# Optimization experiments

Hardware: AMD Instinct MI355X
Metric: run time of the kernel (lower is better)

## Reference

```python
import jax, jax.numpy as jnp
import numpy as np

B, N, E, K, DI, DO = 16, 1024, 16, 3, 32, 32


def setup_inputs() -> dict:
    key = jax.random.key(0)
    k1, k2, k3, k4, k5 = jax.random.split(key, 5)
    return {
        "x": jax.random.normal(k1, (B, N, DI), dtype=jnp.float32),
        "all_emb": jax.random.normal(k2, (B, N, E), dtype=jnp.float32),
        "stock_emb": jax.random.normal(k3, (B, N, E), dtype=jnp.float32),
        "weights_pool": jax.random.normal(k4, (E, K, DI, DO), dtype=jnp.float32) * 0.1,
        "bias_pool": jax.random.normal(k5, (E, DO), dtype=jnp.float32) * 0.1,
    }


def reference(x, all_emb, stock_emb, weights_pool, bias_pool):
    # dynamic adjacency: relu(E E^T) then row softmax -> [B, N, N]
    A = jax.nn.relu(jnp.einsum('bne,bme->bnm', all_emb, all_emb))
    S = jax.nn.softmax(A, axis=-1)
    b, n, _ = S.shape
    k_orders = weights_pool.shape[1]
    eye = jnp.broadcast_to(jnp.eye(n, dtype=S.dtype), S.shape)
    # Chebyshev recursion T_0 = I, T_1 = S, T_k = 2 S T_{k-1} - T_{k-2}
    supports = [eye, S]
    for _ in range(2, k_orders):
        supports.append(2.0 * jnp.matmul(S, supports[-1]) - supports[-2])
    cheby = jnp.stack(supports, axis=1)  # [B, K, N, N]
    # graph propagation per Chebyshev order: [B, K, N, dim_in]
    x_g = jnp.einsum('bkij,bjd->bkid', cheby, x)
    # node-specific weights from stock_emb, fused with conv (avoids [B,N,K,I,O]):
    # original: weights = einsum('bni,ikop->bnkop'); out = einsum('bkni,bnkio->bnko').sum(k)
    out = jnp.einsum('bkni,bne,ekio->bno', x_g, stock_emb, weights_pool)
    bias = jnp.einsum('bne,eo->bno', stock_emb, bias_pool)
    return out + bias
```

## Files before the change

### kernel.cpp

```cpp
#include <hip/hip_runtime.h>
#include <stdint.h>

typedef __bf16 bf16x8 __attribute__((ext_vector_type(8)));
typedef __bf16 bf16x4 __attribute__((ext_vector_type(4)));
typedef float  f32x16 __attribute__((ext_vector_type(16)));

constexpr int kB = 16;
constexpr int kN = 1024;
constexpr int kE = 16;

struct bfhl { __bf16 h, l; };
__device__ __forceinline__ bfhl hilo(float v) {
    bfhl r;
    r.h = (__bf16)v;
    r.l = (__bf16)(v - (float)r.h);
    return r;
}

__global__ __launch_bounds__(256) void prep(
    const float* __restrict__ emb, const float* __restrict__ x,
    const float* __restrict__ Wp,
    __bf16* __restrict__ es, __bf16* __restrict__ vt1,
    __bf16* __restrict__ xgb, __bf16* __restrict__ wq)
{
    __shared__ float ls[64 * 33];
    const int tid = threadIdx.x;
    const int bid = blockIdx.x;

    if (bid < 256) {
        int c = bid * 256 + tid;
        int row = c >> 2, seg = c & 3;
        float4 v = *(const float4*)(emb + (size_t)c * 4);
        float f[4] = {v.x, v.y, v.z, v.w};
        bf16x4 hi, lo;
        #pragma unroll
        for (int i = 0; i < 4; ++i) { bfhl t = hilo(f[i]); hi[i] = t.h; lo[i] = t.l; }
        __bf16* r = es + (size_t)row * 32;
        *(bf16x4*)(r + seg * 4)      = hi;
        *(bf16x4*)(r + 16 + seg * 4) = lo;
    } else if (bid < 512) {
        const int bb = bid - 256;
        const int b = bb >> 4, n0 = (bb & 15) << 6;
        const float* sB = x + ((size_t)b * kN + n0) * 32;
        #pragma unroll
        for (int it = 0; it < 2; ++it) {
            int f = it * 256 + tid;
            int row = f >> 3, q8 = f & 7;
            float4 v = *(const float4*)(sB + (size_t)row * 32 + q8 * 4);
            ls[row * 33 + q8 * 4 + 0] = v.x;
            ls[row * 33 + q8 * 4 + 1] = v.y;
            ls[row * 33 + q8 * 4 + 2] = v.z;
            ls[row * 33 + q8 * 4 + 3] = v.w;
        }
        __syncthreads();
        if (tid < 128) {
            const int d = (tid >> 2) & 31, ng = tid & 3;
            bf16x8 o0, o1;
            #pragma unroll
            for (int i = 0; i < 16; ++i) {
                __bf16 hcast = (__bf16)ls[(ng * 16 + i) * 33 + d];
                if (i < 8) o0[i] = hcast; else o1[i - 8] = hcast;
            }
            __bf16* dp = vt1 + (size_t)b * 65536 + (size_t)d * 1024 + n0 + ng * 16;
            *(bf16x8*)dp       = o0;
            *(bf16x8*)(dp + 8) = o1;
        }
        {
            const int r2 = tid >> 2, jg = tid & 3;
            bf16x8 hi, lo;
            #pragma unroll
            for (int i = 0; i < 8; ++i) {
                bfhl t = hilo(ls[r2 * 33 + jg * 8 + i]);
                hi[i] = t.h; lo[i] = t.l;
            }
            __bf16* dp = xgb + (size_t)(b * kN + n0 + r2) * 192 + jg * 8;
            *(bf16x8*)dp        = hi;
            *(bf16x8*)(dp + 96) = lo;
        }
    } else {
        int idx = (bid - 512) * 256 + tid;
        if (idx < 6144) {
            int e = idx / 384, rem = idx - e * 384;
            int ks = rem / 64, r2 = rem - ks * 64;
            int o = r2 >> 1, h = r2 & 1;
            int ki0 = ks * 16 + h * 8;
            bf16x8 hi;
            #pragma unroll
            for (int j = 0; j < 8; ++j)
                hi[j] = (__bf16)Wp[(size_t)e * 3072 + (size_t)(ki0 + j) * 32 + o];
            *(bf16x8*)(wq + (size_t)(e * 6 + ks) * 512 + o * 16 + h * 8) = hi;
        }
    }
}

template<int STAGE>
__global__ __launch_bounds__(256, 2) void apply_mfma(
    const __bf16* __restrict__ es,
    const __bf16* __restrict__ vtin,
    const float*  __restrict__ x,
    __bf16* __restrict__ vt2,
    __bf16* __restrict__ xgb)
{
    __shared__ __bf16 es_s[256 * 40];
    __shared__ __bf16 vt_s[32 * 264];
    __shared__ float  ps[4 * 32 * 33];
    __shared__ float  Ls[4 * 32];
    __shared__ float  yb[32 * 33];

    const int tid = threadIdx.x;
    const int w = tid >> 6, l = tid & 63;
    const int q = l & 31, h = l >> 5;
    const int b = blockIdx.x >> 5, q0 = (blockIdx.x & 31) << 5;

    const __bf16* esB = es + (size_t)b * 32768;
    const __bf16* vtB = vtin + (size_t)b * 65536;

    const __bf16* qr = esB + (size_t)(q0 + q) * 32;
    bf16x8 bhi = *(const bf16x8*)(qr + 8 * h);
    bf16x8 blo = *(const bf16x8*)(qr + 16 + 8 * h);

    f32x16 acc = {};
    float Lp = 0.f;

    for (int ch = 0; ch < 4; ++ch) {
        __syncthreads();
        #pragma unroll
        for (int i = 0; i < 4; ++i) {
            int f = i * 256 + tid;
            int rl = f >> 2, c = f & 3;
            bf16x8 v = *(const bf16x8*)(esB + (size_t)(ch * 256 + rl) * 32 + c * 8);
            *(bf16x8*)(es_s + rl * 40 + c * 8) = v;
        }
        #pragma unroll
        for (int it = 0; it < 2; ++it) {
            int G = it * 256 + tid;
            int d = G >> 4, g = G & 15;
            const __bf16* src = vtB + (size_t)d * 1024 + ch * 256 + g * 16;
            bf16x8 in0 = *(const bf16x8*)src;
            bf16x8 in1 = *(const bf16x8*)(src + 8);
            bf16x8 out0 = __builtin_shufflevector(in0, in1, 0, 1, 2, 3, 8, 9, 10, 11);
            bf16x8 out1 = __builtin_shufflevector(in0, in1, 4, 5, 6, 7, 12, 13, 14, 15);
            *(bf16x8*)(vt_s + d * 264 + g * 16)     = out0;
            *(bf16x8*)(vt_s + d * 264 + g * 16 + 8) = out1;
        }
        __syncthreads();

        #pragma unroll
        for (int sub = 0; sub < 2; ++sub) {
            const int kbl = (w << 6) + (sub << 5);
            const __bf16* ar = es_s + (size_t)(kbl + q) * 40;
            bf16x8 ahi = *(const bf16x8*)(ar + 8 * h);
            bf16x8 alo = *(const bf16x8*)(ar + 16 + 8 * h);

            f32x16 S = {};
            S = __builtin_amdgcn_mfma_f32_32x32x16_bf16(ahi, bhi, S, 0, 0, 0);
            S = __builtin_amdgcn_mfma_f32_32x32x16_bf16(ahi, blo, S, 0, 0, 0);
            S = __builtin_amdgcn_mfma_f32_32x32x16_bf16(alo, bhi, S, 0, 0, 0);

            float p[16];
            #pragma unroll
            for (int r = 0; r < 16; ++r) {
                p[r] = __expf(fmaxf(S[r], 0.f));
                Lp += p[r];
            }
            bf16x8 P0, P1;
            #pragma unroll
            for (int j = 0; j < 8; ++j) { P0[j] = (__bf16)p[j]; P1[j] = (__bf16)p[8 + j]; }

            const __bf16* vh = vt_s + (size_t)q * 264 + kbl;
            bf16x8 A0 = *(const bf16x8*)(vh + 8 * h);
            bf16x8 A1 = *(const bf16x8*)(vh + 16 + 8 * h);
            acc = __builtin_amdgcn_mfma_f32_32x32x16_bf16(A0, P0, acc, 0, 0, 0);
            acc = __builtin_amdgcn_mfma_f32_32x32x16_bf16(A1, P1, acc, 0, 0, 0);
        }
    }

    Lp += __shfl_xor(Lp, 32);
    #pragma unroll
    for (int r = 0; r < 16; ++r) {
        int d = (r & 3) + 8 * (r >> 2) + 4 * h;
        ps[w * 1056 + d * 33 + q] = acc[r];
    }
    if (l < 32) Ls[w * 32 + l] = Lp;
    __syncthreads();

    const int qq = tid >> 3, dg = tid & 7;
    const float iL = 1.f / (Ls[qq] + Ls[32 + qq] + Ls[64 + qq] + Ls[96 + qq]);
    float yv[4];
    #pragma unroll
    for (int i = 0; i < 4; ++i) {
        int d = dg * 4 + i;
        yv[i] = (ps[d * 33 + qq] + ps[1056 + d * 33 + qq] +
                 ps[2112 + d * 33 + qq] + ps[3168 + d * 33 + qq]) * iL;
    }

    {
        float src[4];
        if (STAGE == 2) {
            float4 xv = *(const float4*)(x + (size_t)(b * kN + q0 + qq) * 32 + dg * 4);
            src[0] = 2.f * yv[0] - xv.x; src[1] = 2.f * yv[1] - xv.y;
            src[2] = 2.f * yv[2] - xv.z; src[3] = 2.f * yv[3] - xv.w;
        } else {
            #pragma unroll
            for (int i = 0; i < 4; ++i) src[i] = yv[i];
        }
        const int koff = (STAGE == 1) ? 32 : 64;
        bf16x4 hi, lo;
        #pragma unroll
        for (int i = 0; i < 4; ++i) { bfhl t = hilo(src[i]); hi[i] = t.h; lo[i] = t.l; }
        __bf16* dp = xgb + (size_t)(b * kN + q0 + qq) * 192 + koff + dg * 4;
        *(bf16x4*)dp        = hi;
        *(bf16x4*)(dp + 96) = lo;
    }

    if (STAGE == 1) {
        #pragma unroll
        for (int i = 0; i < 4; ++i) yb[qq * 33 + dg * 4 + i] = yv[i];
        __syncthreads();
        const int d = tid >> 3, qg = tid & 7;
        bf16x4 hi;
        #pragma unroll
        for (int i = 0; i < 4; ++i) hi[i] = (__bf16)yb[(qg * 4 + i) * 33 + d];
        *(bf16x4*)(vt2 + (size_t)b * 65536 + (size_t)d * 1024 + q0 + qg * 4) = hi;
    }
}

__global__ __launch_bounds__(256, 2) void final_mfma(
    const __bf16* __restrict__ xgb,
    const float*  __restrict__ stock,
    const __bf16* __restrict__ wq,
    const float*  __restrict__ bias,
    float* __restrict__ out)
{
    __shared__ __bf16 xga[2 * 32 * 104];
    __shared__ float  s_s[32 * 16];
    __shared__ float  ps[4 * 32 * 33];

    const int tid = threadIdx.x;
    const int w = tid >> 6, l = tid & 63;
    const int o = l & 31, h = l >> 5;
    const int n0 = blockIdx.x << 5;

    #pragma unroll
    for (int it = 0; it < 3; ++it) {
        int c = it * 256 + tid;
        int n = c / 24, r = c - n * 24;
        int pl = r / 12, s12 = r - pl * 12;
        bf16x8 v = *(const bf16x8*)(xgb + (size_t)(n0 + n) * 192 + pl * 96 + s12 * 8);
        *(bf16x8*)(xga + pl * 3328 + n * 104 + s12 * 8) = v;
    }
    {
        int r = tid >> 3, e2 = (tid & 7) * 2;
        *(float2*)(s_s + r * 16 + e2) = *(const float2*)(stock + (size_t)(n0 + r) * 16 + e2);
    }
    __syncthreads();

    f32x16 acc[4] = {};
    const int e0 = w * 4;

    #pragma unroll
    for (int ks = 0; ks < 6; ++ks) {
        bf16x8 Ah = *(const bf16x8*)(xga + o * 104 + ks * 16 + 8 * h);
        bf16x8 Al = *(const bf16x8*)(xga + 3328 + o * 104 + ks * 16 + 8 * h);
        #pragma unroll
        for (int ei = 0; ei < 4; ++ei) {
            bf16x8 Bh = *(const bf16x8*)(wq + (size_t)((e0 + ei) * 6 + ks) * 512 + o * 16 + h * 8);
            acc[ei] = __builtin_amdgcn_mfma_f32_32x32x16_bf16(Ah, Bh, acc[ei], 0, 0, 0);
            acc[ei] = __builtin_amdgcn_mfma_f32_32x32x16_bf16(Al, Bh, acc[ei], 0, 0, 0);
        }
    }

    float pr[16];
    #pragma unroll
    for (int r = 0; r < 16; ++r) pr[r] = 0.f;
    #pragma unroll
    for (int ei = 0; ei < 4; ++ei) {
        const int eg = e0 + ei;
        const float bv = bias[eg * 32 + o];
        #pragma unroll
        for (int r = 0; r < 16; ++r) {
            int node = (r & 3) + 8 * (r >> 2) + 4 * h;
            pr[r] += s_s[node * 16 + eg] * (acc[ei][r] + bv);
        }
    }
    #pragma unroll
    for (int r = 0; r < 16; ++r) {
        int node = (r & 3) + 8 * (r >> 2) + 4 * h;
        ps[w * 1056 + node * 33 + o] = pr[r];
    }
    __syncthreads();
    {
        const int node = tid >> 3, og = (tid & 7) * 4;
        float4 s;
        #pragma unroll
        for (int i = 0; i < 4; ++i) {
            int c = node * 33 + og + i;
            ((float*)&s)[i] = ps[c] + ps[1056 + c] + ps[2112 + c] + ps[3168 + c];
        }
        *(float4*)(out + (size_t)(n0 + node) * 32 + og) = s;
    }
}

extern "C" void kernel_launch(void* const* d_in, const int* in_sizes, int n_in,
                              void* d_out, int out_size, void* d_ws, size_t ws_size,
                              hipStream_t stream) {
    const float* x     = (const float*)d_in[0];
    const float* aemb  = (const float*)d_in[1];
    const float* stock = (const float*)d_in[2];
    const float* Wp    = (const float*)d_in[3];
    const float* bias  = (const float*)d_in[4];
    float* out = (float*)d_out;

    float*  ws  = (float*)d_ws;
    __bf16* es  = (__bf16*)ws;
    __bf16* vt1 = (__bf16*)(ws + 262144);
    __bf16* vt2 = (__bf16*)(ws + 786432);
    __bf16* xgb = (__bf16*)(ws + 1310720);
    __bf16* wq  = (__bf16*)(ws + 2883584);

    prep<<<dim3(536), dim3(256), 0, stream>>>(aemb, x, Wp, es, vt1, xgb, wq);
    apply_mfma<1><<<dim3(512), dim3(256), 0, stream>>>(es, vt1, x, vt2, xgb);
    apply_mfma<2><<<dim3(512), dim3(256), 0, stream>>>(es, vt2, x, vt2, xgb);
    final_mfma<<<dim3(512), dim3(256), 0, stream>>>(xgb, stock, wq, bias, out);
}
```

Measured before the change: 33.37 us.

## Store operands in MFMA-fragment layout, drop LDS staging, fuse final into stage 2

Prep and stage 1 now write embeddings, transposed x/y and the hi/lo Chebyshev features directly in the per-lane MFMA fragment order. The apply kernel can then load fragments straight from global memory, with no LDS staging loops or block barriers in the main loop. The final projection kernel is folded into stage 2: T2 is kept in shared memory and combined with the stored T0/T1 fragments, which removes one launch and a global round trip. The cost is more uncoalesced-looking direct global loads per wave and a longer stage-2 kernel.

```diff
diff --git a/kernel.cpp b/kernel.cpp
--- a/kernel.cpp
+++ b/kernel.cpp
@@ -7,7 +7,6 @@
 
 constexpr int kB = 16;
 constexpr int kN = 1024;
-constexpr int kE = 16;
 
 struct bfhl { __bf16 h, l; };
 __device__ __forceinline__ bfhl hilo(float v) {
@@ -17,27 +16,35 @@
     return r;
 }
 
+__device__ __forceinline__ int moff(int f, int h, int j) {
+    return 16 * f + ((j < 4) ? (4 * h + j) : (4 * h + j + 4));
+}
+
+
 __global__ __launch_bounds__(256) void prep(
     const float* __restrict__ emb, const float* __restrict__ x,
     const float* __restrict__ Wp,
-    __bf16* __restrict__ es, __bf16* __restrict__ vt1,
-    __bf16* __restrict__ xgb, __bf16* __restrict__ wq)
+    __bf16* __restrict__ esf, __bf16* __restrict__ vtf1,
+    __bf16* __restrict__ xgf, __bf16* __restrict__ wq)
 {
-    __shared__ float ls[64 * 33];
+    __shared__ float ls[64 * 36];
     const int tid = threadIdx.x;
     const int bid = blockIdx.x;
 
     if (bid < 256) {
-        int c = bid * 256 + tid;
-        int row = c >> 2, seg = c & 3;
-        float4 v = *(const float4*)(emb + (size_t)c * 4);
+        const int b = bid >> 4, rg = (bid & 15) << 6;
+        const int r = tid >> 2, seg = tid & 3;
+        float4 v = *(const float4*)(emb + ((size_t)(b * kN + rg + r) * 16 + seg * 4));
         float f[4] = {v.x, v.y, v.z, v.w};
         bf16x4 hi, lo;
         #pragma unroll
         for (int i = 0; i < 4; ++i) { bfhl t = hilo(f[i]); hi[i] = t.h; lo[i] = t.l; }
-        __bf16* r = es + (size_t)row * 32;
-        *(bf16x4*)(r + seg * 4)      = hi;
-        *(bf16x4*)(r + 16 + seg * 4) = lo;
+        const int kt = ((bid & 15) << 1) + (r >> 5);
+        const int lane = ((seg >> 1) << 5) + (r & 31);
+        const int j0 = (seg & 1) << 2;
+        __bf16* base = esf + ((size_t)(b * 32 + kt) * 2) * 512 + lane * 8 + j0;
+        *(bf16x4*)base         = hi;
+        *(bf16x4*)(base + 512) = lo;
     } else if (bid < 512) {
         const int bb = bid - 256;
         const int b = bb >> 4, n0 = (bb & 15) << 6;
@@ -47,35 +54,34 @@
             int f = it * 256 + tid;
             int row = f >> 3, q8 = f & 7;
             float4 v = *(const float4*)(sB + (size_t)row * 32 + q8 * 4);
-            ls[row * 33 + q8 * 4 + 0] = v.x;
-            ls[row * 33 + q8 * 4 + 1] = v.y;
-            ls[row * 33 + q8 * 4 + 2] = v.z;
-            ls[row * 33 + q8 * 4 + 3] = v.w;
+            *(float4*)(&ls[row * 36 + q8 * 4]) = v;
         }
         __syncthreads();
-        if (tid < 128) {
-            const int d = (tid >> 2) & 31, ng = tid & 3;
-            bf16x8 o0, o1;
-            #pragma unroll
-            for (int i = 0; i < 16; ++i) {
-                __bf16 hcast = (__bf16)ls[(ng * 16 + i) * 33 + d];
-                if (i < 8) o0[i] = hcast; else o1[i - 8] = hcast;
-            }
-            __bf16* dp = vt1 + (size_t)b * 65536 + (size_t)d * 1024 + n0 + ng * 16;
-            *(bf16x8*)dp       = o0;
-            *(bf16x8*)(dp + 8) = o1;
-        }
         {
-            const int r2 = tid >> 2, jg = tid & 3;
-            bf16x8 hi, lo;
-            #pragma unroll
-            for (int i = 0; i < 8; ++i) {
-                bfhl t = hilo(ls[r2 * 33 + jg * 8 + i]);
-                hi[i] = t.h; lo[i] = t.l;
-            }
-            __bf16* dp = xgb + (size_t)(b * kN + n0 + r2) * 192 + jg * 8;
-            *(bf16x8*)dp        = hi;
-            *(bf16x8*)(dp + 96) = lo;
+            const int mt = tid >> 7, fr = (tid >> 6) & 1, l = tid & 63;
+            const int d = l & 31, h = l >> 5;
+            bf16x8 ov;
+            #pragma unroll
+            for (int j = 0; j < 8; ++j)
+                ov[j] = (__bf16)ls[(mt * 32 + moff(fr, h, j)) * 36 + d];
+            *(bf16x8*)(vtf1 + ((size_t)(b * 32 + (n0 >> 5) + mt) * 2 + fr) * 512 + l * 8) = ov;
+        }
+        #pragma unroll
+        for (int mt = 0; mt < 2; ++mt) {
+            const int ks = tid >> 7, pl = (tid >> 6) & 1, l = tid & 63;
+            const int node = l & 31, h = l >> 5;
+            const float* rp = &ls[(mt * 32 + node) * 36 + ks * 16 + 8 * h];
+            float4 u0 = *(const float4*)rp;
+            float4 u1 = *(const float4*)(rp + 4);
+            float u[8] = {u0.x, u0.y, u0.z, u0.w, u1.x, u1.y, u1.z, u1.w};
+            bf16x8 ov;
+            #pragma unroll
+            for (int j = 0; j < 8; ++j) {
+                bfhl t = hilo(u[j]);
+                ov[j] = pl ? t.l : t.h;
+            }
+            const int ntile = b * 32 + (n0 >> 5) + mt;
+            *(bf16x8*)(xgf + ((size_t)(ntile * 4 + ks) * 2 + pl) * 512 + l * 8) = ov;
         }
     } else {
         int idx = (bid - 512) * 256 + tid;
@@ -95,84 +101,69 @@
 
 template<int STAGE>
 __global__ __launch_bounds__(256, 2) void apply_mfma(
-    const __bf16* __restrict__ es,
+    const __bf16* __restrict__ esf,
     const __bf16* __restrict__ vtin,
     const float*  __restrict__ x,
-    __bf16* __restrict__ vt2,
-    __bf16* __restrict__ xgb)
+    __bf16* __restrict__ vtout,
+    __bf16* __restrict__ xgf,
+    const __bf16* __restrict__ wq,
+    const float*  __restrict__ stock,
+    const float*  __restrict__ bias,
+    float* __restrict__ out)
 {
-    __shared__ __bf16 es_s[256 * 40];
-    __shared__ __bf16 vt_s[32 * 264];
-    __shared__ float  ps[4 * 32 * 33];
-    __shared__ float  Ls[4 * 32];
-    __shared__ float  yb[32 * 33];
+    __shared__ alignas(16) char smem[24576];
+    float*  ps  = (float*)smem;
+    float*  Ls  = (float*)(smem + 16896);
+    float*  yb  = (float*)(smem + 17408);
+    __bf16* xg2 = (__bf16*)(smem + 17408);
+    float*  s_s = (float*)(smem + 22016);
 
     const int tid = threadIdx.x;
     const int w = tid >> 6, l = tid & 63;
     const int q = l & 31, h = l >> 5;
     const int b = blockIdx.x >> 5, q0 = (blockIdx.x & 31) << 5;
-
-    const __bf16* esB = es + (size_t)b * 32768;
-    const __bf16* vtB = vtin + (size_t)b * 65536;
-
-    const __bf16* qr = esB + (size_t)(q0 + q) * 32;
-    bf16x8 bhi = *(const bf16x8*)(qr + 8 * h);
-    bf16x8 blo = *(const bf16x8*)(qr + 16 + 8 * h);
+    const int ntile = blockIdx.x;
+
+    const __bf16* esfB = esf + (size_t)b * 32768;
+    const __bf16* vtfB = vtin + (size_t)b * 32768;
+
+    if (STAGE == 2) {
+        int r = tid >> 3, e2 = (tid & 7) * 2;
+        *(float2*)(s_s + r * 16 + e2) =
+            *(const float2*)(stock + (size_t)(b * kN + q0 + r) * 16 + e2);
+    }
+
+    bf16x8 bhi = *(const bf16x8*)(esfB + ((size_t)(q0 >> 5) * 2) * 512 + l * 8);
+    bf16x8 blo = *(const bf16x8*)(esfB + ((size_t)(q0 >> 5) * 2 + 1) * 512 + l * 8);
 
     f32x16 acc = {};
     float Lp = 0.f;
 
-    for (int ch = 0; ch < 4; ++ch) {
-        __syncthreads();
-        #pragma unroll
-        for (int i = 0; i < 4; ++i) {
-            int f = i * 256 + tid;
-            int rl = f >> 2, c = f & 3;
-            bf16x8 v = *(const bf16x8*)(esB + (size_t)(ch * 256 + rl) * 32 + c * 8);
-            *(bf16x8*)(es_s + rl * 40 + c * 8) = v;
-        }
-        #pragma unroll
-        for (int it = 0; it < 2; ++it) {
-            int G = it * 256 + tid;
-            int d = G >> 4, g = G & 15;
-            const __bf16* src = vtB + (size_t)d * 1024 + ch * 256 + g * 16;
-            bf16x8 in0 = *(const bf16x8*)src;
-            bf16x8 in1 = *(const bf16x8*)(src + 8);
-            bf16x8 out0 = __builtin_shufflevector(in0, in1, 0, 1, 2, 3, 8, 9, 10, 11);
-            bf16x8 out1 = __builtin_shufflevector(in0, in1, 4, 5, 6, 7, 12, 13, 14, 15);
-            *(bf16x8*)(vt_s + d * 264 + g * 16)     = out0;
-            *(bf16x8*)(vt_s + d * 264 + g * 16 + 8) = out1;
-        }
-        __syncthreads();
-
-        #pragma unroll
-        for (int sub = 0; sub < 2; ++sub) {
-            const int kbl = (w << 6) + (sub << 5);
-            const __bf16* ar = es_s + (size_t)(kbl + q) * 40;
-            bf16x8 ahi = *(const bf16x8*)(ar + 8 * h);
-            bf16x8 alo = *(const bf16x8*)(ar + 16 + 8 * h);
-
-            f32x16 S = {};
-            S = __builtin_amdgcn_mfma_f32_32x32x16_bf16(ahi, bhi, S, 0, 0, 0);
-            S = __builtin_amdgcn_mfma_f32_32x32x16_bf16(ahi, blo, S, 0, 0, 0);
-            S = __builtin_amdgcn_mfma_f32_32x32x16_bf16(alo, bhi, S, 0, 0, 0);
-
-            float p[16];
-            #pragma unroll
-            for (int r = 0; r < 16; ++r) {
-                p[r] = __expf(fmaxf(S[r], 0.f));
-                Lp += p[r];
-            }
-            bf16x8 P0, P1;
-            #pragma unroll
-            for (int j = 0; j < 8; ++j) { P0[j] = (__bf16)p[j]; P1[j] = (__bf16)p[8 + j]; }
-
-            const __bf16* vh = vt_s + (size_t)q * 264 + kbl;
-            bf16x8 A0 = *(const bf16x8*)(vh + 8 * h);
-            bf16x8 A1 = *(const bf16x8*)(vh + 16 + 8 * h);
-            acc = __builtin_amdgcn_mfma_f32_32x32x16_bf16(A0, P0, acc, 0, 0, 0);
-            acc = __builtin_amdgcn_mfma_f32_32x32x16_bf16(A1, P1, acc, 0, 0, 0);
-        }
+    #pragma unroll 2
+    for (int it = 0; it < 8; ++it) {
+        const int kt = it * 4 + w;
+        bf16x8 ahi = *(const bf16x8*)(esfB + ((size_t)kt * 2) * 512 + l * 8);
+        bf16x8 alo = *(const bf16x8*)(esfB + ((size_t)kt * 2 + 1) * 512 + l * 8);
+        bf16x8 A0  = *(const bf16x8*)(vtfB + ((size_t)kt * 2) * 512 + l * 8);
+        bf16x8 A1  = *(const bf16x8*)(vtfB + ((size_t)kt * 2 + 1) * 512 + l * 8);
+
+        f32x16 S = {};
+        S = __builtin_amdgcn_mfma_f32_32x32x16_bf16(ahi, bhi, S, 0, 0, 0);
+        S = __builtin_amdgcn_mfma_f32_32x32x16_bf16(ahi, blo, S, 0, 0, 0);
+        S = __builtin_amdgcn_mfma_f32_32x32x16_bf16(alo, bhi, S, 0, 0, 0);
+
+        float p[16];
+        #pragma unroll
+        for (int r = 0; r < 16; ++r) {
+            p[r] = __expf(fmaxf(S[r], 0.f));
+            Lp += p[r];
+        }
+        bf16x8 P0, P1;
+        #pragma unroll
+        for (int j = 0; j < 8; ++j) { P0[j] = (__bf16)p[j]; P1[j] = (__bf16)p[8 + j]; }
+
+        acc = __builtin_amdgcn_mfma_f32_32x32x16_bf16(A0, P0, acc, 0, 0, 0);
+        acc = __builtin_amdgcn_mfma_f32_32x32x16_bf16(A1, P1, acc, 0, 0, 0);
     }
 
     Lp += __shfl_xor(Lp, 32);
@@ -194,110 +185,106 @@
                  ps[2112 + d * 33 + qq] + ps[3168 + d * 33 + qq]) * iL;
     }
 
-    {
-        float src[4];
-        if (STAGE == 2) {
+    if (STAGE == 1) {
+        #pragma unroll
+        for (int i = 0; i < 4; ++i) yb[qq * 36 + dg * 4 + i] = yv[i];
+        __syncthreads();
+        if (tid < 128) {
+            const int fr = tid >> 6, l2 = tid & 63;
+            const int d = l2 & 31, h2 = l2 >> 5;
+            bf16x8 ov;
+            #pragma unroll
+            for (int j = 0; j < 8; ++j)
+                ov[j] = (__bf16)yb[moff(fr, h2, j) * 36 + d];
+            *(bf16x8*)(vtout + ((size_t)(b * 32 + (q0 >> 5)) * 2 + fr) * 512 + l2 * 8) = ov;
+        }
+        {
+            const int ks2 = tid >> 7, pl = (tid >> 6) & 1, l2 = tid & 63;
+            const int node = l2 & 31, h2 = l2 >> 5;
+            const float* rp = &yb[node * 36 + ks2 * 16 + 8 * h2];
+            float4 u0 = *(const float4*)rp;
+            float4 u1 = *(const float4*)(rp + 4);
+            float u[8] = {u0.x, u0.y, u0.z, u0.w, u1.x, u1.y, u1.z, u1.w};
+            bf16x8 ov;
+            #pragma unroll
+            for (int j = 0; j < 8; ++j) {
+                bfhl t = hilo(u[j]);
+                ov[j] = pl ? t.l : t.h;
+            }
+            *(bf16x8*)(xgf + ((size_t)(ntile * 4 + 2 + ks2) * 2 + pl) * 512 + l2 * 8) = ov;
+        }
+    } else {
+        {
             float4 xv = *(const float4*)(x + (size_t)(b * kN + q0 + qq) * 32 + dg * 4);
-            src[0] = 2.f * yv[0] - xv.x; src[1] = 2.f * yv[1] - xv.y;
-            src[2] = 2.f * yv[2] - xv.z; src[3] = 2.f * yv[3] - xv.w;
-        } else {
-            #pragma unroll
-            for (int i = 0; i < 4; ++i) src[i] = yv[i];
-        }
-        const int koff = (STAGE == 1) ? 32 : 64;
-        bf16x4 hi, lo;
-        #pragma unroll
-        for (int i = 0; i < 4; ++i) { bfhl t = hilo(src[i]); hi[i] = t.h; lo[i] = t.l; }
-        __bf16* dp = xgb + (size_t)(b * kN + q0 + qq) * 192 + koff + dg * 4;
-        *(bf16x4*)dp        = hi;
-        *(bf16x4*)(dp + 96) = lo;
-    }
-
-    if (STAGE == 1) {
-        #pragma unroll
-        for (int i = 0; i < 4; ++i) yb[qq * 33 + dg * 4 + i] = yv[i];
+            float g[4] = {2.f * yv[0] - xv.x, 2.f * yv[1] - xv.y,
+                          2.f * yv[2] - xv.z, 2.f * yv[3] - xv.w};
+            bf16x4 hi, lo;
+            #pragma unroll
+            for (int i = 0; i < 4; ++i) { bfhl t = hilo(g[i]); hi[i] = t.h; lo[i] = t.l; }
+            *(bf16x4*)(xg2 + qq * 36 + dg * 4)        = hi;
+            *(bf16x4*)(xg2 + 1152 + qq * 36 + dg * 4) = lo;
+        }
         __syncthreads();
-        const int d = tid >> 3, qg = tid & 7;
-        bf16x4 hi;
-        #pragma unroll
-        for (int i = 0; i < 4; ++i) hi[i] = (__bf16)yb[(qg * 4 + i) * 33 + d];
-        *(bf16x4*)(vt2 + (size_t)b * 65536 + (size_t)d * 1024 + q0 + qg * 4) = hi;
-    }
-}
-
-__global__ __launch_bounds__(256, 2) void final_mfma(
-    const __bf16* __restrict__ xgb,
-    const float*  __restrict__ stock,
-    const __bf16* __restrict__ wq,
-    const float*  __restrict__ bias,
-    float* __restrict__ out)
-{
-    __shared__ __bf16 xga[2 * 32 * 104];
-    __shared__ float  s_s[32 * 16];
-    __shared__ float  ps[4 * 32 * 33];
-
-    const int tid = threadIdx.x;
-    const int w = tid >> 6, l = tid & 63;
-    const int o = l & 31, h = l >> 5;
-    const int n0 = blockIdx.x << 5;
-
-    #pragma unroll
-    for (int it = 0; it < 3; ++it) {
-        int c = it * 256 + tid;
-        int n = c / 24, r = c - n * 24;
-        int pl = r / 12, s12 = r - pl * 12;
-        bf16x8 v = *(const bf16x8*)(xgb + (size_t)(n0 + n) * 192 + pl * 96 + s12 * 8);
-        *(bf16x8*)(xga + pl * 3328 + n * 104 + s12 * 8) = v;
-    }
-    {
-        int r = tid >> 3, e2 = (tid & 7) * 2;
-        *(float2*)(s_s + r * 16 + e2) = *(const float2*)(stock + (size_t)(n0 + r) * 16 + e2);
-    }
-    __syncthreads();
-
-    f32x16 acc[4] = {};
-    const int e0 = w * 4;
-
-    #pragma unroll
-    for (int ks = 0; ks < 6; ++ks) {
-        bf16x8 Ah = *(const bf16x8*)(xga + o * 104 + ks * 16 + 8 * h);
-        bf16x8 Al = *(const bf16x8*)(xga + 3328 + o * 104 + ks * 16 + 8 * h);
+
+        f32x16 acc2[4] = {};
+        const int e0 = w * 4;
+        const int o = q;
+
+        #pragma unroll
+        for (int ks = 0; ks < 6; ++ks) {
+            bf16x8 Ah, Al;
+            if (ks < 4) {
+                Ah = *(const bf16x8*)(xgf + ((size_t)(ntile * 4 + ks) * 2) * 512 + l * 8);
+                Al = *(const bf16x8*)(xgf + ((size_t)(ntile * 4 + ks) * 2 + 1) * 512 + l * 8);
+            } else {
+                const int base = o * 36 + (ks - 4) * 16 + 8 * h;
+                bf16x4 a0 = *(const bf16x4*)(xg2 + base);
+                bf16x4 a1 = *(const bf16x4*)(xg2 + base + 4);
+                bf16x4 b0 = *(const bf16x4*)(xg2 + 1152 + base);
+                bf16x4 b1 = *(const bf16x4*)(xg2 + 1152 + base + 4);
+                #pragma unroll
+                for (int j = 0; j < 4; ++j) {
+                    Ah[j] = a0[j]; Ah[4 + j] = a1[j];
+                    Al[j] = b0[j]; Al[4 + j] = b1[j];
+                }
+            }
+            #pragma unroll
+            for (int ei = 0; ei < 4; ++ei) {
+                bf16x8 Bh = *(const bf16x8*)(wq + (size_t)((e0 + ei) * 6 + ks) * 512 + o * 16 + h * 8);
+                acc2[ei] = __builtin_amdgcn_mfma_f32_32x32x16_bf16(Ah, Bh, acc2[ei], 0, 0, 0);
+                acc2[ei] = __builtin_amdgcn_mfma_f32_32x32x16_bf16(Al, Bh, acc2[ei], 0, 0, 0);
+            }
+        }
+
+        float pr[16];
+        #pragma unroll
+        for (int r = 0; r < 16; ++r) pr[r] = 0.f;
         #pragma unroll
         for (int ei = 0; ei < 4; ++ei) {
-            bf16x8 Bh = *(const bf16x8*)(wq + (size_t)((e0 + ei) * 6 + ks) * 512 + o * 16 + h * 8);
-            acc[ei] = __builtin_amdgcn_mfma_f32_32x32x16_bf16(Ah, Bh, acc[ei], 0, 0, 0);
-            acc[ei] = __builtin_amdgcn_mfma_f32_32x32x16_bf16(Al, Bh, acc[ei], 0, 0, 0);
-        }
-    }
-
-    float pr[16];
-    #pragma unroll
-    for (int r = 0; r < 16; ++r) pr[r] = 0.f;
-    #pragma unroll
-    for (int ei = 0; ei < 4; ++ei) {
-        const int eg = e0 + ei;
-        const float bv = bias[eg * 32 + o];
+            const int eg = e0 + ei;
+            const float bv = bias[eg * 32 + o];
+            #pragma unroll
+            for (int r = 0; r < 16; ++r) {
+                int node = (r & 3) + 8 * (r >> 2) + 4 * h;
+                pr[r] += s_s[node * 16 + eg] * (acc2[ei][r] + bv);
+            }
+        }
         #pragma unroll
         for (int r = 0; r < 16; ++r) {
             int node = (r & 3) + 8 * (r >> 2) + 4 * h;
-            pr[r] += s_s[node * 16 + eg] * (acc[ei][r] + bv);
-        }
-    }
-    #pragma unroll
-    for (int r = 0; r < 16; ++r) {
-        int node = (r & 3) + 8 * (r >> 2) + 4 * h;
-        ps[w * 1056 + node * 33 + o] = pr[r];
-    }
-    __syncthreads();
-    {
-        const int node = tid >> 3, og = (tid & 7) * 4;
-        float4 s;
-        #pragma unroll
-        for (int i = 0; i < 4; ++i) {
-            int c = node * 33 + og + i;
-            ((float*)&s)[i] = ps[c] + ps[1056 + c] + ps[2112 + c] + ps[3168 + c];
-        }
-        *(float4*)(out + (size_t)(n0 + node) * 32 + og) = s;
+            ps[w * 1056 + node * 33 + o] = pr[r];
+        }
+        __syncthreads();
+        {
+            const int node = tid >> 3, og = (tid & 7) * 4;
+            float4 s;
+            #pragma unroll
+            for (int i = 0; i < 4; ++i) {
+                int c = node * 33 + og + i;
+                ((float*)&s)[i] = ps[c] + ps[1056 + c] + ps[2112 + c] + ps[3168 + c];
+            }
+            *(float4*)(out + (size_t)(b * kN + q0 + node) * 32 + og) = s;
+        }
     }
 }
 
@@ -311,15 +298,16 @@
     const float* bias  = (const float*)d_in[4];
     float* out = (float*)d_out;
 
-    float*  ws  = (float*)d_ws;
-    __bf16* es  = (__bf16*)ws;
-    __bf16* vt1 = (__bf16*)(ws + 262144);
-    __bf16* vt2 = (__bf16*)(ws + 786432);
-    __bf16* xgb = (__bf16*)(ws + 1310720);
-    __bf16* wq  = (__bf16*)(ws + 2883584);
-
-    prep<<<dim3(536), dim3(256), 0, stream>>>(aemb, x, Wp, es, vt1, xgb, wq);
-    apply_mfma<1><<<dim3(512), dim3(256), 0, stream>>>(es, vt1, x, vt2, xgb);
-    apply_mfma<2><<<dim3(512), dim3(256), 0, stream>>>(es, vt2, x, vt2, xgb);
-    final_mfma<<<dim3(512), dim3(256), 0, stream>>>(xgb, stock, wq, bias, out);
-}
+    __bf16* wsb  = (__bf16*)d_ws;
+    __bf16* esf  = wsb;
+    __bf16* vtf1 = wsb + 524288;
+    __bf16* vtf2 = wsb + 1048576;
+    __bf16* xgf  = wsb + 1572864;
+    __bf16* wq   = wsb + 3670016;
+
+    prep<<<dim3(536), dim3(256), 0, stream>>>(aemb, x, Wp, esf, vtf1, xgf, wq);
+    apply_mfma<1><<<dim3(512), dim3(256), 0, stream>>>(
+        esf, vtf1, x, vtf2, xgf, wq, stock, bias, out);
+    apply_mfma<2><<<dim3(512), dim3(256), 0, stream>>>(
+        esf, vtf2, x, nullptr, xgf, wq, stock, bias, out);
+}
```

Result: faster. 29.10 us (-12.8%).
